# Kernel tuning notes

Hardware: AMD Instinct MI355X
Metric: run time of the kernel (lower is better)

Reference implementation:

```python
import jax, jax.numpy as jnp
import numpy as np

N = 8192
D_IN = 1024
D_OUT = 1024


def setup_inputs() -> dict:
    key = jax.random.key(0)
    ks = jax.random.split(key, 7)
    s = 1.0 / np.sqrt(D_IN)
    return {
        "feat": jax.random.normal(ks[0], (N, D_IN), dtype=jnp.float32),
        "Wq": jax.random.uniform(ks[1], (D_IN, D_OUT), jnp.float32, -s, s),
        "bq": jax.random.uniform(ks[2], (D_OUT,), jnp.float32, -s, s),
        "Wk": jax.random.uniform(ks[3], (D_IN, D_OUT), jnp.float32, -s, s),
        "bk": jax.random.uniform(ks[4], (D_OUT,), jnp.float32, -s, s),
        "Wv": jax.random.uniform(ks[5], (D_IN, D_OUT), jnp.float32, -s, s),
        "bv": jax.random.uniform(ks[6], (D_OUT,), jnp.float32, -s, s),
    }


def reference(feat, Wq, bq, Wk, bk, Wv, bv):
    # eval mode: dropout(p=0.3, training=False) is identity
    q = feat @ Wq + bq          # [N, D_OUT]
    k = feat @ Wk + bk          # [N, D_OUT]
    v = feat @ Wv + bv          # [N, D_OUT]
    scale = 1.0 / jnp.sqrt(jnp.float32(D_OUT))
    scores = (q @ k.T) * scale  # [N, N]
    attn = jax.nn.softmax(scores, axis=1)
    return attn @ v             # [N, D_OUT]
```

## Files before the change

kernel.cpp:

```cpp
#include <hip/hip_runtime.h>
#include <hip/hip_bf16.h>
#include <stdint.h>

typedef __hip_bfloat16 bf16;
typedef __attribute__((ext_vector_type(8))) short short8;
typedef __attribute__((ext_vector_type(4))) float f32x4;

#define BM 128
#define BN 128

__device__ __forceinline__ unsigned short f2bf_bits(float x) {
    return __builtin_bit_cast(unsigned short, __float2bfloat16(x));
}

__device__ __forceinline__ void gload_lds16(const bf16* g, bf16* l) {
    __builtin_amdgcn_global_load_lds(
        (const __attribute__((address_space(1))) void*)(const void*)g,
        (__attribute__((address_space(3))) void*)(void*)l,
        16, 0, 0);
}

template <int N>
__device__ __forceinline__ void waitvm() {
    if constexpr (N == 0) asm volatile("s_waitcnt vmcnt(0)" ::: "memory");
    else if constexpr (N == 4) asm volatile("s_waitcnt vmcnt(4)" ::: "memory");
    else if constexpr (N == 6) asm volatile("s_waitcnt vmcnt(6)" ::: "memory");
}

__global__ void prep_kernel(const float* __restrict__ feat, unsigned short* __restrict__ featb,
                            const float* __restrict__ W0, const float* __restrict__ W1,
                            const float* __restrict__ W2, bf16* __restrict__ Wt,
                            float* __restrict__ lsum) {
    const int b = blockIdx.x;
    const int tid = threadIdx.x;
    if (b < 8192) {
        int i = b * 256 + tid;
        float4 v = reinterpret_cast<const float4*>(feat)[i];
        ushort4 o;
        o.x = f2bf_bits(v.x); o.y = f2bf_bits(v.y);
        o.z = f2bf_bits(v.z); o.w = f2bf_bits(v.w);
        reinterpret_cast<ushort4*>(featb)[i] = o;
    } else if (b < 11264) {
        __shared__ float tile[32][33];
        const int b2 = b - 8192;
        const int z = b2 >> 10;
        const int t = b2 & 1023;
        const int bx = t & 31, by = t >> 5;
        const int tx = tid & 31, ty = tid >> 5;
        const float* in = (z == 0) ? W0 : (z == 1) ? W1 : W2;
        bf16* out = Wt + (size_t)z * 1024 * 1024;
        for (int r = ty; r < 32; r += 8)
            tile[r][tx] = in[(size_t)(by * 32 + r) * 1024 + bx * 32 + tx];
        __syncthreads();
        for (int r = ty; r < 32; r += 8)
            out[(size_t)(bx * 32 + r) * 1024 + by * 32 + tx] = __float2bfloat16(tile[tx][r]);
    } else {
        for (int i = tid; i < 8192; i += 256) lsum[i] = 0.f;
    }
}

__global__ void scale_rows(float* __restrict__ out, const float* __restrict__ lsum) {
    int i = blockIdx.x * 256 + threadIdx.x;
    float4 v = reinterpret_cast<float4*>(out)[i];
    float inv = 1.0f / lsum[i >> 8];
    v.x *= inv; v.y *= inv; v.z *= inv; v.w *= inv;
    reinterpret_cast<float4*>(out)[i] = v;
}

template <int MODE, int KH, int SWAP>
__global__ __launch_bounds__(256, 4)
void gemm_bt(const bf16* __restrict__ A, const bf16* __restrict__ B,
             const float* __restrict__ b0, const float* __restrict__ b1,
             const float* __restrict__ b2, float* __restrict__ lsum,
             bf16* __restrict__ outb, float* __restrict__ outf,
             int M, int N, int K, int ldb, int ldout, float scale) {
    constexpr int TILE = 128 * 32;
    constexpr int SELEMS = (2 * KH * TILE < 9216) ? 9216 : 2 * KH * TILE;
    __shared__ bf16 smem[SELEMS];
    bf16* As = smem;
    bf16* Bs = smem + KH * TILE;

    const int tid  = threadIdx.x;
    const int lane = tid & 63;
    const int wave = tid >> 6;
    const int wm = wave & 1, wn = wave >> 1;
    const int l16  = lane & 15;
    const int quad = lane >> 4;
    long bm0, bn0;
    if (SWAP == 2) {
        const int lin = blockIdx.y * 8 + blockIdx.x;
        const int xcd = lin & 7;
        const int s   = lin >> 3;
        bn0 = (long)(s & 7) * BN;
        bm0 = (long)((s >> 3) * 8 + xcd) * BM;
    } else {
        bm0 = (long)(SWAP ? blockIdx.y : blockIdx.x) * BM;
        bn0 = (long)(SWAP ? blockIdx.x : blockIdx.y) * BN;
    }

    const bf16* Ause = A;
    const bf16* Buse = B;
    bf16* oz = outb;
    int  ldo = ldout;
    int  z   = 0;
    if (MODE == 0) {
        z = blockIdx.z;
        if (z == 2) {
            bm0  = (long)blockIdx.y * BM;
            bn0  = (long)blockIdx.x * BN;
            Ause = B + (size_t)2 * N * K;
            Buse = A;
            oz   = outb + (size_t)2 * M * ldout;
            ldo  = M;
        } else {
            Buse = B + (size_t)z * N * K;
            oz   = outb + (size_t)z * M * ldout;
        }
    }

    const int lrow = lane >> 2;
    const int lcol = (lane & 3) * 8;
    const bf16* gA[2][KH];
    const bf16* gB[2][KH];
    bf16* lA[2][KH];
    bf16* lB[2][KH];
#pragma unroll
    for (int u = 0; u < 2; u++)
#pragma unroll
        for (int h = 0; h < KH; h++) {
            gA[u][h] = Ause + (size_t)(bm0 + wave * 32 + u * 16 + lrow) * K + h * 32 + lcol;
            gB[u][h] = Buse + (size_t)(bn0 + wave * 32 + u * 16 + lrow) * ldb + h * 32 + lcol;
            lA[u][h] = As + h * TILE + (wave * 32 + u * 16) * 32;
            lB[u][h] = Bs + h * TILE + (wave * 32 + u * 16) * 32;
        }

    const bf16* Ard = As + (wm * 64 + l16) * 32 + quad * 8;
    const bf16* Brd = Bs + (wn * 64 + l16) * 32 + quad * 8;

    f32x4 acc[4][4];
    const f32x4 zero = {0.f, 0.f, 0.f, 0.f};
#pragma unroll
    for (int i = 0; i < 4; i++)
#pragma unroll
        for (int j = 0; j < 4; j++) acc[i][j] = zero;

    for (int k0 = 0; k0 < K; k0 += KH * 32) {
        __syncthreads();
#pragma unroll
        for (int u = 0; u < 2; u++)
#pragma unroll
            for (int h = 0; h < KH; h++) {
                gload_lds16(gA[u][h] + k0, lA[u][h]);
                gload_lds16(gB[u][h] + k0, lB[u][h]);
            }
        __syncthreads();
#pragma unroll
        for (int h = 0; h < KH; h++) {
            short8 af[4], bfr[4];
#pragma unroll
            for (int mi = 0; mi < 4; mi++)
                af[mi] = *reinterpret_cast<const short8*>(Ard + h * TILE + mi * 16 * 32);
#pragma unroll
            for (int ni = 0; ni < 4; ni++)
                bfr[ni] = *reinterpret_cast<const short8*>(Brd + h * TILE + ni * 16 * 32);
#pragma unroll
            for (int mi = 0; mi < 4; mi++)
#pragma unroll
                for (int ni = 0; ni < 4; ni++)
                    acc[mi][ni] = __builtin_amdgcn_mfma_f32_16x16x32_bf16(af[mi], bfr[ni], acc[mi][ni], 0, 0, 0);
        }
    }

    if (MODE == 0 || MODE == 1) {
        __syncthreads();
        float bcol[4];
        if (MODE == 0 && z < 2) {
            const float* bias = (z == 0) ? b0 : b1;
#pragma unroll
            for (int ni = 0; ni < 4; ni++) bcol[ni] = bias[bn0 + wn * 64 + l16 + ni * 16];
        }
#pragma unroll
        for (int mi = 0; mi < 4; mi++) {
            bf16* eb = smem + ((wave << 1) | (mi & 1)) * 1152;
#pragma unroll
            for (int r = 0; r < 4; r++) {
                float s = 0.f;
                float brow = 0.f;
                if (MODE == 0 && z == 2) brow = b2[bm0 + wm * 64 + mi * 16 + quad * 4 + r];
#pragma unroll
                for (int ni = 0; ni < 4; ni++) {
                    float v = acc[mi][ni][r];
                    if (MODE == 0) v += (z == 2) ? brow : bcol[ni];
                    else { v = __expf(v * scale); s += v; }
                    eb[(quad * 4 + r) * 72 + ni * 16 + l16] = __float2bfloat16(v);
                }
                if (MODE == 1) {
                    s += __shfl_xor(s, 1);
                    s += __shfl_xor(s, 2);
                    s += __shfl_xor(s, 4);
                    s += __shfl_xor(s, 8);
                    if (l16 == 0) atomicAdd(&lsum[bm0 + wm * 64 + mi * 16 + quad * 4 + r], s);
                }
            }
            asm volatile("s_waitcnt lgkmcnt(0)" ::: "memory");
#pragma unroll
            for (int p = 0; p < 2; p++) {
                int r2 = p * 8 + (lane >> 3);
                int c2 = (lane & 7) * 8;
                short8 val = *reinterpret_cast<const short8*>(eb + r2 * 72 + c2);
                *reinterpret_cast<short8*>(
                    oz + (size_t)(bm0 + wm * 64 + mi * 16 + r2) * ldo + bn0 + wn * 64 + c2) = val;
            }
        }
    } else {
        const int rb2 = wm * 64 + quad * 4;
        const int cb2 = wn * 64 + l16;
#pragma unroll
        for (int mi = 0; mi < 4; mi++)
#pragma unroll
            for (int r = 0; r < 4; r++) {
                long row = bm0 + rb2 + mi * 16 + r;
                float mul = (MODE == 3) ? 1.0f / lsum[row] : 0.f;
#pragma unroll
                for (int ni = 0; ni < 4; ni++) {
                    long col = bn0 + cb2 + ni * 16;
                    if (MODE == 3) outf[row * ldout + col] = acc[mi][ni][r] * mul;
                    else           outf[row * ldout + col] += acc[mi][ni][r];
                }
            }
    }
}

__global__ __launch_bounds__(512, 1)
void gemm8q(const bf16* __restrict__ A, const bf16* __restrict__ B,
            float* __restrict__ lsum, bf16* __restrict__ outb,
            int K, int ldout, float scale) {
    __shared__ __align__(16) bf16 smem[8 * 8192];

    const int tid  = threadIdx.x;
    const int lane = tid & 63;
    const int w    = tid >> 6;
    const int wm   = w >> 2;
    const int wn   = w & 3;
    const int l16  = lane & 15;
    const int quad = lane >> 4;

    const int bid = blockIdx.x;
    const int s   = (bid & 7) * 128 + (bid >> 3);
    const long bm0 = (long)(s >> 5) * 256;
    const long bn0 = (long)(s & 31) * 256;

    const int srow = lane >> 3;
    const int scol = ((lane & 7) ^ srow) * 8;
    const bf16* gAs[2][2];
    const bf16* gBs[2][2];
#pragma unroll
    for (int h = 0; h < 2; h++)
#pragma unroll
        for (int c = 0; c < 2; c++) {
            gAs[h][c] = A + (size_t)(bm0 + h * 128 + c * 64 + w * 8 + srow) * K + scol;
            gBs[h][c] = B + (size_t)(bn0 + h * 128 + c * 64 + w * 8 + srow) * K + scol;
        }
    auto stg = [&](const bf16* const* src, int mh, int u) {
        bf16* base = smem + (size_t)((((u & 1) << 2) | mh) * 8192) + w * 512;
        gload_lds16(src[0] + (size_t)u * 64, base);
        gload_lds16(src[1] + (size_t)u * 64, base + 4096);
    };

    const int swzb = (l16 & 7) << 4;
    int colE[2];
#pragma unroll
    for (int ks = 0; ks < 2; ks++)
        colE[ks] = ((ks * 64 + quad * 16) ^ swzb) >> 1;
    const int arow = l16;
    const int brow = (wn & 1) * 64 + l16;
    const int slA = (0 << 1) | wm;
    const int slB = (1 << 1) | (wn >> 1);

    const int T = K / 64;

    f32x4 acc[8][4];
    const f32x4 zero = {0.f, 0.f, 0.f, 0.f};
#pragma unroll
    for (int i = 0; i < 8; i++)
#pragma unroll
        for (int j = 0; j < 4; j++) acc[i][j] = zero;

    stg(gAs[0], 0, 0); stg(gAs[1], 1, 0); stg(gBs[0], 2, 0); stg(gBs[1], 3, 0);
    stg(gAs[0], 0, 1); stg(gBs[0], 2, 1); stg(gBs[1], 3, 1);
    waitvm<6>();
    __builtin_amdgcn_s_barrier();

    for (int u = 0; u < T; ++u) {
        const bf16* sa = smem + (size_t)((((u & 1) << 2) | slA) * 8192);
        const bf16* sb = smem + (size_t)((((u & 1) << 2) | slB) * 8192);
        short8 bfr[2][4];
#pragma unroll
        for (int r = 0; r < 4; ++r) {
            short8 af[2][2];
            if (r == 0) {
#pragma unroll
                for (int ks = 0; ks < 2; ks++)
#pragma unroll
                    for (int ni = 0; ni < 4; ni++)
                        bfr[ks][ni] = *reinterpret_cast<const short8*>(
                            sb + (brow + ni * 16) * 64 + colE[ks]);
            }
#pragma unroll
            for (int j = 0; j < 2; j++)
#pragma unroll
                for (int ks = 0; ks < 2; ks++)
                    af[j][ks] = *reinterpret_cast<const short8*>(
                        sa + ((r * 2 + j) * 16 + arow) * 64 + colE[ks]);
            if (r == 0) asm volatile("s_waitcnt lgkmcnt(8)" ::: "memory");
            __builtin_amdgcn_s_barrier();
            asm volatile("s_waitcnt lgkmcnt(0)" ::: "memory");
            __builtin_amdgcn_sched_barrier(0);
            __builtin_amdgcn_s_setprio(1);
#pragma unroll
            for (int j = 0; j < 2; j++)
#pragma unroll
                for (int ks = 0; ks < 2; ks++)
#pragma unroll
                    for (int ni = 0; ni < 4; ni++)
                        acc[r * 2 + j][ni] = __builtin_amdgcn_mfma_f32_16x16x32_bf16(
                            af[j][ks], bfr[ks][ni], acc[r * 2 + j][ni], 0, 0, 0);
            __builtin_amdgcn_s_setprio(0);
            __builtin_amdgcn_s_barrier();
            if (r == 0) {
                if (u + 1 < T) stg(gAs[1], 1, u + 1);
                if (u + 2 < T) stg(gBs[0], 2, u + 2);
            } else if (r == 1) {
                if (u + 2 < T) stg(gBs[1], 3, u + 2);
            } else if (r == 2) {
                if (u + 2 < T)      waitvm<4>();
                else if (u + 1 < T) waitvm<0>();
            } else {
                if (u + 2 < T) stg(gAs[0], 0, u + 2);
            }
        }
    }
    __syncthreads();

#pragma unroll
    for (int mi = 0; mi < 8; mi++) {
        bf16* eb = smem + ((w << 1) | (mi & 1)) * 1152;
#pragma unroll
        for (int r = 0; r < 4; r++) {
            float ssum = 0.f;
#pragma unroll
            for (int ni = 0; ni < 4; ni++) {
                float v = __expf(acc[mi][ni][r] * scale);
                ssum += v;
                eb[(quad * 4 + r) * 72 + ni * 16 + l16] = __float2bfloat16(v);
            }
            ssum += __shfl_xor(ssum, 1);
            ssum += __shfl_xor(ssum, 2);
            ssum += __shfl_xor(ssum, 4);
            ssum += __shfl_xor(ssum, 8);
            if (l16 == 0)
                atomicAdd(&lsum[bm0 + wm * 128 + mi * 16 + quad * 4 + r], ssum);
        }
        asm volatile("s_waitcnt lgkmcnt(0)" ::: "memory");
#pragma unroll
        for (int p = 0; p < 2; p++) {
            int r2 = p * 8 + (lane >> 3);
            int c2 = (lane & 7) * 8;
            short8 val = *reinterpret_cast<const short8*>(eb + r2 * 72 + c2);
            *reinterpret_cast<short8*>(
                outb + (size_t)(bm0 + wm * 128 + mi * 16 + r2) * ldout + bn0 + wn * 64 + c2) = val;
        }
    }
}

extern "C" void kernel_launch(void* const* d_in, const int* in_sizes, int n_in,
                              void* d_out, int out_size, void* d_ws, size_t ws_size,
                              hipStream_t stream) {
    const float* feat = (const float*)d_in[0];
    const float* Wq   = (const float*)d_in[1];
    const float* bqv  = (const float*)d_in[2];
    const float* Wk   = (const float*)d_in[3];
    const float* bkv  = (const float*)d_in[4];
    const float* Wv   = (const float*)d_in[5];
    const float* bvv  = (const float*)d_in[6];
    float* outp = (float*)d_out;

    const int M = 8192, D = 1024;
    char* ws = (char*)d_ws;
    size_t off = 0;
    auto carve = [&](size_t bytes) -> char* {
        char* r = ws + off;
        off += (bytes + 255) & ~(size_t)255;
        return r;
    };
    bf16* featb = (bf16*)carve((size_t)M * D * 2);
    bf16* Wbt   = (bf16*)carve((size_t)3 * D * D * 2);
    bf16* qk    = (bf16*)carve((size_t)2 * M * D * 2 + (size_t)D * M * 2);
    bf16* vbt   = qk + (size_t)2 * M * D;
    float* lsum = (float*)carve((size_t)M * 4);
    size_t avail = (ws_size > off) ? ws_size - off : 0;

    int C;
    if      (avail >= (size_t)M * M * 2)    C = M;
    else if (avail >= (size_t)M * 4096 * 2) C = 4096;
    else if (avail >= (size_t)M * 2048 * 2) C = 2048;
    else                                    C = 1024;
    bf16* Pc = (bf16*)carve((size_t)M * C * 2);

    prep_kernel<<<dim3(11265), dim3(256), 0, stream>>>(
        feat, (unsigned short*)featb, Wq, Wk, Wv, Wbt, lsum);
    gemm_bt<0, 2, 0><<<dim3(M / 128, D / 128, 3), dim3(256), 0, stream>>>(
        featb, Wbt, bqv, bkv, bvv, nullptr, qk, nullptr, M, D, D, D, D, 1.0f);

    const float scale = 0.03125f;
    bf16* qb = qk;
    bf16* kb = qk + (size_t)M * D;
    if (C == M) {
        gemm8q<<<dim3(1024), dim3(512), 0, stream>>>(
            qb, kb, lsum, Pc, D, M, scale);
        gemm_bt<3, 2, 2><<<dim3(D / 128, M / 128), dim3(256), 0, stream>>>(
            Pc, vbt, nullptr, nullptr, nullptr, lsum, nullptr, outp, M, D, M, M, D, 0.f);
    } else {
        hipMemsetAsync(outp, 0, (size_t)M * D * 4, stream);
        for (int c = 0; c < M / C; c++) {
            gemm_bt<1, 2, 0><<<dim3(M / 128, C / 128), dim3(256), 0, stream>>>(
                qb, kb + (size_t)c * C * D, nullptr, nullptr, nullptr, lsum, Pc, nullptr,
                M, C, D, D, C, scale);
            gemm_bt<2, 2, 1><<<dim3(D / 128, M / 128), dim3(256), 0, stream>>>(
                Pc, vbt + (size_t)c * C, nullptr, nullptr, nullptr, nullptr, nullptr, outp,
                M, D, C, M, D, 0.f);
        }
        scale_rows<<<dim3(M * D / 4 / 256), dim3(256), 0, stream>>>(outp, lsum);
    }
}
```

Measured before the change: 502.0 us.

## Move specialized 8-wave kernel from QK^T scores to the P·V GEMM

Measured after the change: 441.9 us. 1.14x faster.

```diff
diff --git a/kernel.cpp b/kernel.cpp
--- a/kernel.cpp
+++ b/kernel.cpp
@@ -23,7 +23,6 @@
 template <int N>
 __device__ __forceinline__ void waitvm() {
     if constexpr (N == 0) asm volatile("s_waitcnt vmcnt(0)" ::: "memory");
-    else if constexpr (N == 4) asm volatile("s_waitcnt vmcnt(4)" ::: "memory");
     else if constexpr (N == 6) asm volatile("s_waitcnt vmcnt(6)" ::: "memory");
 }
 
@@ -232,145 +231,139 @@
 }
 
 __global__ __launch_bounds__(512, 1)
-void gemm8q(const bf16* __restrict__ A, const bf16* __restrict__ B,
-            float* __restrict__ lsum, bf16* __restrict__ outb,
-            int K, int ldout, float scale) {
-    __shared__ __align__(16) bf16 smem[8 * 8192];
+void gemm8v(const bf16* __restrict__ A, const bf16* __restrict__ B,
+            const float* __restrict__ lsum, float* __restrict__ outf,
+            int K, int lda, int ldb, int ldout) {
+    constexpr int SLOT = (256 + 128) * 64;
+    __shared__ __align__(16) bf16 smem[3 * SLOT];
 
     const int tid  = threadIdx.x;
     const int lane = tid & 63;
     const int w    = tid >> 6;
-    const int wm   = w >> 2;
-    const int wn   = w & 3;
+    const int wm   = w >> 1;
+    const int wn   = w & 1;
     const int l16  = lane & 15;
     const int quad = lane >> 4;
-
-    const int bid = blockIdx.x;
-    const int s   = (bid & 7) * 128 + (bid >> 3);
-    const long bm0 = (long)(s >> 5) * 256;
-    const long bn0 = (long)(s & 31) * 256;
-
-    const int srow = lane >> 3;
-    const int scol = ((lane & 7) ^ srow) * 8;
-    const bf16* gAs[2][2];
-    const bf16* gBs[2][2];
-#pragma unroll
-    for (int h = 0; h < 2; h++)
-#pragma unroll
-        for (int c = 0; c < 2; c++) {
-            gAs[h][c] = A + (size_t)(bm0 + h * 128 + c * 64 + w * 8 + srow) * K + scol;
-            gBs[h][c] = B + (size_t)(bn0 + h * 128 + c * 64 + w * 8 + srow) * K + scol;
-        }
-    auto stg = [&](const bf16* const* src, int mh, int u) {
-        bf16* base = smem + (size_t)((((u & 1) << 2) | mh) * 8192) + w * 512;
-        gload_lds16(src[0] + (size_t)u * 64, base);
-        gload_lds16(src[1] + (size_t)u * 64, base + 4096);
+    const int xr   = l16 & 7;
+
+    const int lin = blockIdx.y * 8 + blockIdx.x;
+    const int xcd = lin & 7;
+    const int s   = lin >> 3;
+    const long bn0 = (long)(s & 7) * 128;
+    const long bm0 = (long)((s >> 3) * 8 + xcd) * 256;
+
+    const int grow = lane >> 3;
+    const int gcol = ((lane & 7) ^ grow) * 8;
+    const bf16* gAsrc[4];
+    const bf16* gBsrc[2];
+    int ldsA[4], ldsB[2];
+#pragma unroll
+    for (int j = 0; j < 4; j++) {
+        gAsrc[j] = A + (size_t)(bm0 + (w * 4 + j) * 8 + grow) * lda + gcol;
+        ldsA[j]  = (w * 4 + j) * 8 * 64;
+    }
+#pragma unroll
+    for (int j = 0; j < 2; j++) {
+        gBsrc[j] = B + (size_t)(bn0 + (w * 2 + j) * 8 + grow) * ldb + gcol;
+        ldsB[j]  = (256 + (w * 2 + j) * 8) * 64;
+    }
+
+    int aoff[4][2], boff[4][2];
+#pragma unroll
+    for (int mi = 0; mi < 4; mi++)
+#pragma unroll
+        for (int ks = 0; ks < 2; ks++)
+            aoff[mi][ks] = (wm * 64 + mi * 16 + l16) * 64 + (((ks * 4 + quad) ^ xr) * 8);
+#pragma unroll
+    for (int ni = 0; ni < 4; ni++)
+#pragma unroll
+        for (int ks = 0; ks < 2; ks++)
+            boff[ni][ks] = (256 + wn * 64 + ni * 16 + l16) * 64 + (((ks * 4 + quad) ^ xr) * 8);
+
+    f32x4 acc[4][4];
+    const f32x4 zero = {0.f, 0.f, 0.f, 0.f};
+#pragma unroll
+    for (int i = 0; i < 4; i++)
+#pragma unroll
+        for (int j = 0; j < 4; j++) acc[i][j] = zero;
+
+    auto stg = [&](bf16* dst, int u, int part) {
+        size_t ko = (size_t)u * 64;
+        if (part == 0) {
+            gload_lds16(gAsrc[0] + ko, dst + ldsA[0]);
+            gload_lds16(gAsrc[1] + ko, dst + ldsA[1]);
+            gload_lds16(gBsrc[0] + ko, dst + ldsB[0]);
+        } else {
+            gload_lds16(gAsrc[2] + ko, dst + ldsA[2]);
+            gload_lds16(gAsrc[3] + ko, dst + ldsA[3]);
+            gload_lds16(gBsrc[1] + ko, dst + ldsB[1]);
+        }
     };
 
-    const int swzb = (l16 & 7) << 4;
-    int colE[2];
-#pragma unroll
-    for (int ks = 0; ks < 2; ks++)
-        colE[ks] = ((ks * 64 + quad * 16) ^ swzb) >> 1;
-    const int arow = l16;
-    const int brow = (wn & 1) * 64 + l16;
-    const int slA = (0 << 1) | wm;
-    const int slB = (1 << 1) | (wn >> 1);
-
     const int T = K / 64;
-
-    f32x4 acc[8][4];
-    const f32x4 zero = {0.f, 0.f, 0.f, 0.f};
-#pragma unroll
-    for (int i = 0; i < 8; i++)
-#pragma unroll
-        for (int j = 0; j < 4; j++) acc[i][j] = zero;
-
-    stg(gAs[0], 0, 0); stg(gAs[1], 1, 0); stg(gBs[0], 2, 0); stg(gBs[1], 3, 0);
-    stg(gAs[0], 0, 1); stg(gBs[0], 2, 1); stg(gBs[1], 3, 1);
+    stg(smem, 0, 0);            stg(smem, 0, 1);
+    stg(smem + SLOT, 1, 0);     stg(smem + SLOT, 1, 1);
     waitvm<6>();
     __builtin_amdgcn_s_barrier();
 
+    int rs = 0;
     for (int u = 0; u < T; ++u) {
-        const bf16* sa = smem + (size_t)((((u & 1) << 2) | slA) * 8192);
-        const bf16* sb = smem + (size_t)((((u & 1) << 2) | slB) * 8192);
-        short8 bfr[2][4];
-#pragma unroll
-        for (int r = 0; r < 4; ++r) {
+        const bf16* sl = smem + rs * SLOT;
+        int ss = rs + 2; if (ss >= 3) ss -= 3;
+        bf16* sdst = smem + ss * SLOT;
+        const bool doStage = (u + 2 < T);
+
+        short8 bfr[4][2];
+#pragma unroll
+        for (int ph = 0; ph < 2; ++ph) {
             short8 af[2][2];
-            if (r == 0) {
+            if (ph == 0) {
+#pragma unroll
+                for (int ni = 0; ni < 4; ni++)
+#pragma unroll
+                    for (int ks = 0; ks < 2; ks++)
+                        bfr[ni][ks] = *reinterpret_cast<const short8*>(sl + boff[ni][ks]);
+            }
+#pragma unroll
+            for (int j = 0; j < 2; j++)
 #pragma unroll
                 for (int ks = 0; ks < 2; ks++)
-#pragma unroll
-                    for (int ni = 0; ni < 4; ni++)
-                        bfr[ks][ni] = *reinterpret_cast<const short8*>(
-                            sb + (brow + ni * 16) * 64 + colE[ks]);
-            }
-#pragma unroll
-            for (int j = 0; j < 2; j++)
-#pragma unroll
-                for (int ks = 0; ks < 2; ks++)
-                    af[j][ks] = *reinterpret_cast<const short8*>(
-                        sa + ((r * 2 + j) * 16 + arow) * 64 + colE[ks]);
-            if (r == 0) asm volatile("s_waitcnt lgkmcnt(8)" ::: "memory");
+                    af[j][ks] = *reinterpret_cast<const short8*>(sl + aoff[ph * 2 + j][ks]);
+            if (doStage) stg(sdst, u + 2, ph);
+            if (ph == 1 && u + 1 < T) {
+                if (doStage) waitvm<6>();
+                else         waitvm<0>();
+            }
             __builtin_amdgcn_s_barrier();
             asm volatile("s_waitcnt lgkmcnt(0)" ::: "memory");
             __builtin_amdgcn_sched_barrier(0);
             __builtin_amdgcn_s_setprio(1);
 #pragma unroll
-            for (int j = 0; j < 2; j++)
-#pragma unroll
-                for (int ks = 0; ks < 2; ks++)
+            for (int ks = 0; ks < 2; ks++)
+#pragma unroll
+                for (int j = 0; j < 2; j++)
 #pragma unroll
                     for (int ni = 0; ni < 4; ni++)
-                        acc[r * 2 + j][ni] = __builtin_amdgcn_mfma_f32_16x16x32_bf16(
-                            af[j][ks], bfr[ks][ni], acc[r * 2 + j][ni], 0, 0, 0);
+                        acc[ph * 2 + j][ni] = __builtin_amdgcn_mfma_f32_16x16x32_bf16(
+                            af[j][ks], bfr[ni][ks], acc[ph * 2 + j][ni], 0, 0, 0);
             __builtin_amdgcn_s_setprio(0);
             __builtin_amdgcn_s_barrier();
-            if (r == 0) {
-                if (u + 1 < T) stg(gAs[1], 1, u + 1);
-                if (u + 2 < T) stg(gBs[0], 2, u + 2);
-            } else if (r == 1) {
-                if (u + 2 < T) stg(gBs[1], 3, u + 2);
-            } else if (r == 2) {
-                if (u + 2 < T)      waitvm<4>();
-                else if (u + 1 < T) waitvm<0>();
-            } else {
-                if (u + 2 < T) stg(gAs[0], 0, u + 2);
-            }
-        }
-    }
-    __syncthreads();
-
-#pragma unroll
-    for (int mi = 0; mi < 8; mi++) {
-        bf16* eb = smem + ((w << 1) | (mi & 1)) * 1152;
+        }
+        rs = (rs + 1 == 3) ? 0 : rs + 1;
+    }
+
+#pragma unroll
+    for (int mi = 0; mi < 4; mi++)
 #pragma unroll
         for (int r = 0; r < 4; r++) {
-            float ssum = 0.f;
+            long row = bm0 + wm * 64 + mi * 16 + quad * 4 + r;
+            float mul = 1.0f / lsum[row];
 #pragma unroll
             for (int ni = 0; ni < 4; ni++) {
-                float v = __expf(acc[mi][ni][r] * scale);
-                ssum += v;
-                eb[(quad * 4 + r) * 72 + ni * 16 + l16] = __float2bfloat16(v);
-            }
-            ssum += __shfl_xor(ssum, 1);
-            ssum += __shfl_xor(ssum, 2);
-            ssum += __shfl_xor(ssum, 4);
-            ssum += __shfl_xor(ssum, 8);
-            if (l16 == 0)
-                atomicAdd(&lsum[bm0 + wm * 128 + mi * 16 + quad * 4 + r], ssum);
-        }
-        asm volatile("s_waitcnt lgkmcnt(0)" ::: "memory");
-#pragma unroll
-        for (int p = 0; p < 2; p++) {
-            int r2 = p * 8 + (lane >> 3);
-            int c2 = (lane & 7) * 8;
-            short8 val = *reinterpret_cast<const short8*>(eb + r2 * 72 + c2);
-            *reinterpret_cast<short8*>(
-                outb + (size_t)(bm0 + wm * 128 + mi * 16 + r2) * ldout + bn0 + wn * 64 + c2) = val;
-        }
-    }
+                long col = bn0 + wn * 64 + ni * 16 + l16;
+                outf[row * ldout + col] = acc[mi][ni][r] * mul;
+            }
+        }
 }
 
 extern "C" void kernel_launch(void* const* d_in, const int* in_sizes, int n_in,
@@ -416,10 +409,10 @@
     bf16* qb = qk;
     bf16* kb = qk + (size_t)M * D;
     if (C == M) {
-        gemm8q<<<dim3(1024), dim3(512), 0, stream>>>(
-            qb, kb, lsum, Pc, D, M, scale);
-        gemm_bt<3, 2, 2><<<dim3(D / 128, M / 128), dim3(256), 0, stream>>>(
-            Pc, vbt, nullptr, nullptr, nullptr, lsum, nullptr, outp, M, D, M, M, D, 0.f);
+        gemm_bt<1, 2, 0><<<dim3(M / 128, M / 128), dim3(256), 0, stream>>>(
+            qb, kb, nullptr, nullptr, nullptr, lsum, Pc, nullptr, M, M, D, D, M, scale);
+        gemm8v<<<dim3(8, 32), dim3(512), 0, stream>>>(
+            Pc, vbt, lsum, outp, M, M, M, D);
     } else {
         hipMemsetAsync(outp, 0, (size_t)M * D * 4, stream);
         for (int c = 0; c < M / C; c++) {
```
